# Kernel tuning notes

Hardware: AMD Instinct MI355X
Metric: run time of the kernel (lower is better)

## Reference

```python
import jax, jax.numpy as jnp
import numpy as np

L = 0.24          # lambda step size
K = 0.03          # exp(log 0.03), conductance scale used by forward
NITER = 500       # ctor Niter
DEPS = 0.1


def _g(x, k):
    # Perona-Malik conductance: 1 / (1 + |x^2| / k^2); x real so |x*x| == x*x
    return 1.0 / (1.0 + (x * x) / (k * k))


def setup_inputs() -> dict:
    key = jax.random.key(0)
    k1, k2 = jax.random.split(key)
    guide = jax.random.normal(k1, (2, 3, 512, 512), dtype=jnp.float32)
    initial = jax.random.uniform(k2, (2, 1, 512, 512), dtype=jnp.float32)
    return {"guide": guide, "initial": initial}


def reference(guide, initial):
    # shift branch (jit-safe): forward adds deps if initial.min() <= deps, subtracts at end
    shift = jnp.where(jnp.min(initial) <= DEPS, DEPS, 0.0).astype(initial.dtype)
    depth0 = initial + shift

    # conductance coefficients from guide (mean abs channel gradient), shapes:
    # cv: [B,1,H-1,W], ch: [B,1,H,W-1]
    cv = _g(jnp.mean(jnp.abs(guide[:, :, 1:, :] - guide[:, :, :-1, :]), axis=1, keepdims=True), K)
    ch = _g(jnp.mean(jnp.abs(guide[:, :, :, 1:] - guide[:, :, :, :-1]), axis=1, keepdims=True), K)

    def step(I, _):
        # both diffs computed from the same I (matches torch: dv, dh read before writes;
        # the in-place +/- updates commute, so functional adds give identical math)
        dv = I[:, :, 1:, :] - I[:, :, :-1, :]
        dh = I[:, :, :, 1:] - I[:, :, :, :-1]
        tv = L * cv * dv
        th = L * ch * dh
        I = I.at[:, :, 1:, :].add(-tv)
        I = I.at[:, :, :-1, :].add(tv)
        I = I.at[:, :, :, 1:].add(-th)
        I = I.at[:, :, :, :-1].add(th)
        return I, None

    depth, _ = jax.lax.scan(step, depth0, None, length=NITER)
    y_pred = depth - shift
    return (y_pred, cv, ch)
```

## Files before the change

### kernel.cpp

```cpp
#include <hip/hip_runtime.h>


#define HH 512
#define WW 512
#define NB 2
static constexpr float LAM   = 0.24f;
static constexpr float KCOND = 0.03f;
static constexpr float DEPS_ = 0.1f;
static constexpr int IMG      = HH * WW;
static constexpr int N_DEPTH  = NB * IMG;
static constexpr int CV_PER_B = (HH - 1) * WW;
static constexpr int CH_PER_B = HH * (WW - 1);
static constexpr int N_CV     = NB * CV_PER_B;
static constexpr int N_CH     = NB * CH_PER_B;

static constexpr int T_FUSE = 10, NSS = 50;
static constexpr int TILE_W = 64, TILE_H = 32;
static constexpr int HALO_X = 12, HALO_Y = 10;
static constexpr int RW = TILE_W + 2 * HALO_X;
static constexpr int RH = TILE_H + 2 * HALO_Y;
static constexpr int NQ_ROW = RW / 4;
static constexpr int NQUAD  = NQ_ROW * RH;
static constexpr int SSZ    = (RH + 2) * RW;

static constexpr int NU_ROW = RW / 4;
static constexpr int NU_COL = RH / 2;
static constexpr int NUNIT  = NU_ROW * NU_COL;
static constexpr int NTF    = 576;

static constexpr int S_LDS    = 92;
static constexpr int ROWS_SZ  = (RH + 2) * S_LDS;
static constexpr int TRASH_OFF = ROWS_SZ;
static constexpr int EDGE_OFF = ROWS_SZ + S_LDS;
static constexpr int EDGE_ENT = 580;
static constexpr int BUF_SZ   = EDGE_OFF + EDGE_ENT * 4;
static constexpr int MIN_SCR  = TRASH_OFF + 40;

static constexpr int QPT_F = 5;

__device__ __forceinline__ float2 cohload8(const float* p) {
    unsigned long long u = __hip_atomic_load(
        reinterpret_cast<const unsigned long long*>(p),
        __ATOMIC_RELAXED, __HIP_MEMORY_SCOPE_AGENT);
    union { unsigned long long u; float2 f; } c; c.u = u;
    return c.f;
}
__device__ __forceinline__ void cohstore8(float* p, float a, float b) {
    union { unsigned long long u; float f[2]; } c;
    c.f[0] = a; c.f[1] = b;
    __hip_atomic_store(reinterpret_cast<unsigned long long*>(p), c.u,
                       __ATOMIC_RELAXED, __HIP_MEMORY_SCOPE_AGENT);
}

static constexpr int NCO_BLK = (N_CV + N_CH + 255) / 256;
__global__ void coeff_min_kernel(const float* __restrict__ g,
                                 const float* __restrict__ ini,
                                 float* __restrict__ cv, float* __restrict__ chh,
                                 float* __restrict__ partials,
                                 unsigned* __restrict__ flags) {
    constexpr float kk = KCOND * KCOND;
    if ((int)blockIdx.x >= NCO_BLK) {
        int bid = blockIdx.x - NCO_BLK;
        if (threadIdx.x == 0) flags[bid] = 0u;
        float m = 3.4e38f;
        for (int idx = bid * 256 + threadIdx.x; idx < N_DEPTH; idx += 256 * 256)
            m = fminf(m, ini[idx]);
        for (int off = 32; off > 0; off >>= 1) m = fminf(m, __shfl_down(m, off, 64));
        __shared__ float sm[4];
        int lane = threadIdx.x & 63, wv = threadIdx.x >> 6;
        if (lane == 0) sm[wv] = m;
        __syncthreads();
        if (threadIdx.x == 0)
            partials[bid] = fminf(fminf(sm[0], sm[1]), fminf(sm[2], sm[3]));
        return;
    }
    int idx = blockIdx.x * 256 + threadIdx.x;
    if (idx < N_CV) {
        int b = idx / CV_PER_B;
        int r = idx - b * CV_PER_B;
        int i = r >> 9, j = r & (WW - 1);
        const float* gb = g + b * 3 * IMG + i * WW + j;
        float s = 0.f;
#pragma unroll
        for (int c = 0; c < 3; ++c) s += fabsf(gb[c * IMG + WW] - gb[c * IMG]);
        float m = s / 3.0f;
        cv[idx] = 1.0f / (1.0f + (m * m) / kk);
    } else if (idx < N_CV + N_CH) {
        int t = idx - N_CV;
        int b = t / CH_PER_B;
        int r = t - b * CH_PER_B;
        int i = r / (WW - 1);
        int j = r - i * (WW - 1);
        const float* gb = g + b * 3 * IMG + i * WW + j;
        float s = 0.f;
#pragma unroll
        for (int c = 0; c < 3; ++c) s += fabsf(gb[c * IMG + 1] - gb[c * IMG]);
        float m = s / 3.0f;
        chh[t] = 1.0f / (1.0f + (m * m) / kk);
    }
}

__global__ void key_from_partials(const float* __restrict__ partials,
                                  float* __restrict__ keyf) {
    float m = partials[threadIdx.x];
    for (int off = 32; off > 0; off >>= 1) m = fminf(m, __shfl_down(m, off, 64));
    __shared__ float sm[4];
    int lane = threadIdx.x & 63, wv = threadIdx.x >> 6;
    if (lane == 0) sm[wv] = m;
    __syncthreads();
    if (threadIdx.x == 0)
        keyf[0] = fminf(fminf(sm[0], sm[1]), fminf(sm[2], sm[3]));
}

__global__ __launch_bounds__(NTF, 1) void diffuse_persist(
    const float* __restrict__ initial, float* __restrict__ out_y,
    float* __restrict__ bufA, float* __restrict__ bufB,
    const float* __restrict__ cv_g, const float* __restrict__ ch_g,
    const float* __restrict__ partials, unsigned* __restrict__ flags) {
    __shared__ float sb[2][BUF_SZ];
    const int blk = blockIdx.x;
    const int b   = blk >> 7, t = blk & 127;
    const int ty  = t >> 3, tx = t & 7;
    const int y0  = ty * TILE_H;
    const int x0  = tx * TILE_W;
    const int tid = threadIdx.x;

    const bool act = tid < NUNIT;
    const int  uc  = act ? tid : 0;
    const int  pr  = uc / NU_ROW;
    const int  px  = uc - pr * NU_ROW;
    const int  x   = px * 4;
    const int  r0  = 2 * pr, r1 = r0 + 1;
    int roff0 = (r0 + 1) * S_LDS + x;
    int roff1 = roff0 + S_LDS;
    if (!act) { roff0 = TRASH_OFF + (tid & 3) * 8; roff1 = roff0 + 4; }
    const int e_w  = EDGE_OFF + (tid + 1) * 4;
    const int e_lf = EDGE_OFF + tid * 4 + 2;
    const int e_rt = EDGE_OFF + (tid + 2) * 4;

    const int gy0 = y0 - HALO_Y + r0, gy1 = gy0 + 1;
    const int gx  = x0 - HALO_X + x;
    const bool gx_in = (gx >= 0) && (gx <= WW - 4);
    const bool in0 = act && gx_in && (gy0 >= 0) && (gy0 < HH);
    const bool in1 = act && gx_in && (gy1 >= 0) && (gy1 < HH);
    const int goff0 = in0 ? (gy0 * WW + gx) : 0;
    const int goff1 = in1 ? (gy1 * WW + gx) : 0;
    const bool is_int = act && (r0 >= HALO_Y) && (r1 < HALO_Y + TILE_H) &&
                        (x >= HALO_X) && (x < HALO_X + TILE_W);
    const int rel_r = r0 - HALO_Y, rel_x = x - HALO_X;
    const bool is_inner = is_int && (rel_r >= 10) && (rel_r <= 20) &&
                          (rel_x >= 12) && (rel_x <= 48);
    const bool store_seam = is_int && !is_inner;

    const float* cvb = cv_g + b * CV_PER_B;
    const float* chb = ch_g + b * CH_PER_B;
    float ca[4], cm[4], cb[4], h0[5], h1[5];
#pragma unroll
    for (int j = 0; j < 4; ++j) {
        int gxx = gx + j;
        bool gxo = (gxx >= 0) && (gxx < WW);
        bool a_ok = act && (r0 >= 1) && (gy0 >= 1) && (gy0 <= HH - 1) && gxo;
        ca[j] = a_ok ? LAM * cvb[(gy0 - 1) * WW + gxx] : 0.f;
        bool m_ok = act && (gy1 >= 1) && (gy1 <= HH - 1) && gxo;
        cm[j] = m_ok ? LAM * cvb[(gy1 - 1) * WW + gxx] : 0.f;
        bool b_ok = act && (r1 <= RH - 2) && (gy1 + 1 >= 1) && (gy1 + 1 <= HH - 1) && gxo;
        cb[j] = b_ok ? LAM * cvb[gy1 * WW + gxx] : 0.f;
    }
#pragma unroll
    for (int jj = 0; jj < 5; ++jj) {
        int xe = x + jj, gxe = gx + jj;
        bool e_ok = (xe >= 1) && (xe <= RW - 1) && (gxe >= 1) && (gxe < WW);
        bool ok0 = act && e_ok && (gy0 >= 0) && (gy0 < HH);
        h0[jj] = ok0 ? LAM * chb[gy0 * (WW - 1) + (gxe - 1)] : 0.f;
        bool ok1 = act && e_ok && (gy1 >= 0) && (gy1 < HH);
        h1[jj] = ok1 ? LAM * chb[gy1 * (WW - 1) + (gxe - 1)] : 0.f;
    }

    int nbr = -1;
    if (tid < 8) {
        int d  = tid + (tid >= 4 ? 1 : 0);
        int dy = d / 3 - 1, dx = d % 3 - 1;
        int ny = ty + dy, nx = tx + dx;
        if (ny >= 0 && ny < 16 && nx >= 0 && nx < 8)
            nbr = (b << 7) + (ny << 3) + nx;
    }

    float v0[4] = {0.f, 0.f, 0.f, 0.f}, v1[4] = {0.f, 0.f, 0.f, 0.f};
    const float* ib = initial + b * IMG;
    if (in0) {
        float4 tv = *reinterpret_cast<const float4*>(ib + goff0);
        v0[0] = tv.x; v0[1] = tv.y; v0[2] = tv.z; v0[3] = tv.w;
    }
    if (in1) {
        float4 tv = *reinterpret_cast<const float4*>(ib + goff1);
        v1[0] = tv.x; v1[1] = tv.y; v1[2] = tv.z; v1[3] = tv.w;
    }

    {
        float pm = 3.4e38f;
        if (tid < 256) pm = partials[tid];
        for (int off = 32; off > 0; off >>= 1)
            pm = fminf(pm, __shfl_down(pm, off, 64));
        if (tid < 256 && (tid & 63) == 0) sb[0][MIN_SCR + (tid >> 6)] = pm;
    }

    for (int i = tid; i < S_LDS; i += NTF) {
        sb[0][i] = 0.f; sb[0][(RH + 1) * S_LDS + i] = 0.f;
        sb[1][i] = 0.f; sb[1][(RH + 1) * S_LDS + i] = 0.f;
    }
    if (tid == 0) {
        float4 z{0.f, 0.f, 0.f, 0.f};
        *reinterpret_cast<float4*>(&sb[0][EDGE_OFF]) = z;
        *reinterpret_cast<float4*>(&sb[1][EDGE_OFF]) = z;
        *reinterpret_cast<float4*>(&sb[0][EDGE_OFF + 577 * 4]) = z;
        *reinterpret_cast<float4*>(&sb[1][EDGE_OFF + 577 * 4]) = z;
    }
    __syncthreads();

    const float mm = fminf(fminf(sb[0][MIN_SCR], sb[0][MIN_SCR + 1]),
                           fminf(sb[0][MIN_SCR + 2], sb[0][MIN_SCR + 3]));
    const float shift = (mm <= DEPS_) ? DEPS_ : 0.f;
    if (in0) { v0[0] += shift; v0[1] += shift; v0[2] += shift; v0[3] += shift; }
    if (in1) { v1[0] += shift; v1[1] += shift; v1[2] += shift; v1[3] += shift; }

    *reinterpret_cast<float4*>(&sb[0][roff0]) = float4{v0[0], v0[1], v0[2], v0[3]};
    *reinterpret_cast<float4*>(&sb[0][roff1]) = float4{v1[0], v1[1], v1[2], v1[3]};
    *reinterpret_cast<float4*>(&sb[0][e_w])   = float4{v0[0], v1[0], v0[3], v1[3]};
    __syncthreads();

    for (int k = 0; k < NSS; ++k) {
        if (k > 0) {
            if (nbr >= 0) {
                while (__hip_atomic_load(&flags[nbr], __ATOMIC_RELAXED,
                                         __HIP_MEMORY_SCOPE_AGENT) < (unsigned)k) {}
            }
            __syncthreads();
            asm volatile("" ::: "memory");
            const float* srcb = ((k & 1) ? bufA : bufB) + b * IMG;
            if (act && !is_int) {
                float2 a0{0.f, 0.f}, b0{0.f, 0.f}, a1{0.f, 0.f}, b1{0.f, 0.f};
                if (in0) { a0 = cohload8(srcb + goff0); b0 = cohload8(srcb + goff0 + 2); }
                if (in1) { a1 = cohload8(srcb + goff1); b1 = cohload8(srcb + goff1 + 2); }
                v0[0] = a0.x; v0[1] = a0.y; v0[2] = b0.x; v0[3] = b0.y;
                v1[0] = a1.x; v1[1] = a1.y; v1[2] = b1.x; v1[3] = b1.y;
                *reinterpret_cast<float4*>(&sb[0][roff0]) =
                    float4{v0[0], v0[1], v0[2], v0[3]};
                *reinterpret_cast<float4*>(&sb[0][roff1]) =
                    float4{v1[0], v1[1], v1[2], v1[3]};
                *reinterpret_cast<float4*>(&sb[0][e_w]) =
                    float4{v0[0], v1[0], v0[3], v1[3]};
            }
            __syncthreads();
        }

        int cur = 0;
        for (int it = 0; it < T_FUSE; ++it) {
            const float* s = sb[cur];
            float2 lfp = *reinterpret_cast<const float2*>(&s[e_lf]);
            float2 rtp = *reinterpret_cast<const float2*>(&s[e_rt]);
            float4 up = *reinterpret_cast<const float4*>(&s[roff0 - S_LDS]);
            float4 dn = *reinterpret_cast<const float4*>(&s[roff1 + S_LDS]);

            float n0[4], n1[4];
            n0[0] = v0[0] - ca[0] * (v0[0] - up.x) + cm[0] * (v1[0] - v0[0])
                          - h0[0] * (v0[0] - lfp.x) + h0[1] * (v0[1] - v0[0]);
            n0[1] = v0[1] - ca[1] * (v0[1] - up.y) + cm[1] * (v1[1] - v0[1])
                          - h0[1] * (v0[1] - v0[0]) + h0[2] * (v0[2] - v0[1]);
            n0[2] = v0[2] - ca[2] * (v0[2] - up.z) + cm[2] * (v1[2] - v0[2])
                          - h0[2] * (v0[2] - v0[1]) + h0[3] * (v0[3] - v0[2]);
            n0[3] = v0[3] - ca[3] * (v0[3] - up.w) + cm[3] * (v1[3] - v0[3])
                          - h0[3] * (v0[3] - v0[2]) + h0[4] * (rtp.x - v0[3]);
            n1[0] = v1[0] - cm[0] * (v1[0] - v0[0]) + cb[0] * (dn.x - v1[0])
                          - h1[0] * (v1[0] - lfp.y) + h1[1] * (v1[1] - v1[0]);
            n1[1] = v1[1] - cm[1] * (v1[1] - v0[1]) + cb[1] * (dn.y - v1[1])
                          - h1[1] * (v1[1] - v1[0]) + h1[2] * (v1[2] - v1[1]);
            n1[2] = v1[2] - cm[2] * (v1[2] - v0[2]) + cb[2] * (dn.z - v1[2])
                          - h1[2] * (v1[2] - v1[1]) + h1[3] * (v1[3] - v1[2]);
            n1[3] = v1[3] - cm[3] * (v1[3] - v0[3]) + cb[3] * (dn.w - v1[3])
                          - h1[3] * (v1[3] - v1[2]) + h1[4] * (rtp.y - v1[3]);

            int nxt = cur ^ 1;
            float* d = sb[nxt];
            *reinterpret_cast<float4*>(&d[roff0]) = float4{n0[0], n0[1], n0[2], n0[3]};
            *reinterpret_cast<float4*>(&d[roff1]) = float4{n1[0], n1[1], n1[2], n1[3]};
            *reinterpret_cast<float4*>(&d[e_w])   = float4{n0[0], n1[0], n0[3], n1[3]};
            v0[0] = n0[0]; v0[1] = n0[1]; v0[2] = n0[2]; v0[3] = n0[3];
            v1[0] = n1[0]; v1[1] = n1[1]; v1[2] = n1[2]; v1[3] = n1[3];
            cur = nxt;
            __syncthreads();
        }

        if (k == NSS - 1) {
            float* dstb = out_y + b * IMG;
            if (is_int) {
                float4 o0{v0[0] - shift, v0[1] - shift, v0[2] - shift, v0[3] - shift};
                float4 o1{v1[0] - shift, v1[1] - shift, v1[2] - shift, v1[3] - shift};
                *reinterpret_cast<float4*>(dstb + goff0) = o0;
                *reinterpret_cast<float4*>(dstb + goff1) = o1;
            }
        } else {
            float* dstb = ((k & 1) ? bufB : bufA) + b * IMG;
            if (store_seam) {
                cohstore8(dstb + goff0,     v0[0], v0[1]);
                cohstore8(dstb + goff0 + 2, v0[2], v0[3]);
                cohstore8(dstb + goff1,     v1[0], v1[1]);
                cohstore8(dstb + goff1 + 2, v1[2], v1[3]);
            }
            asm volatile("s_waitcnt vmcnt(0)" ::: "memory");
            __syncthreads();
            if (tid == 0)
                __hip_atomic_store(&flags[blk], (unsigned)(k + 1),
                                   __ATOMIC_RELAXED, __HIP_MEMORY_SCOPE_AGENT);
        }
    }
}

template <bool ADD_SHIFT, bool SUB_SHIFT>
__global__ __launch_bounds__(256, 1) void step_fused(
    const float* __restrict__ src, float* __restrict__ dst,
    const float* __restrict__ cv_g, const float* __restrict__ ch_g,
    const float* __restrict__ keyf) {
    __shared__ float sb[2][SSZ];
    const int blk = blockIdx.x;
    const int b = blk >> 7, t = blk & 127;
    const int y0 = (t >> 3) * TILE_H, x0 = (t & 7) * TILE_W;
    const float* cvb = cv_g + b * CV_PER_B;
    const float* chb = ch_g + b * CH_PER_B;
    const float* srcb = src + b * IMG;
    float* dstb = dst + b * IMG;
    float shift = 0.f;
    if (ADD_SHIFT || SUB_SHIFT) shift = (keyf[0] <= DEPS_) ? DEPS_ : 0.f;
    const int tid = threadIdx.x;
    float v[QPT_F][4], cu[QPT_F][4], cd[QPT_F][4], chq[QPT_F][5];
    int roff[QPT_F], rr[QPT_F], xx[QPT_F];
    bool act[QPT_F];
#pragma unroll
    for (int q = 0; q < QPT_F; ++q) {
        int qi = tid + q * 256;
        act[q] = qi < NQUAD;
        int qc = act[q] ? qi : 0;
        int r = qc / NQ_ROW;
        int x = (qc - r * NQ_ROW) * 4;
        rr[q] = r; xx[q] = x;
        roff[q] = (r + 1) * RW + x;
        int gy = y0 - HALO_Y + r, gx = x0 - HALO_X + x;
        bool gy_in = (gy >= 0) && (gy < HH);
#pragma unroll
        for (int j = 0; j < 4; ++j) {
            int gxx = gx + j;
            bool gx_in = (gxx >= 0) && (gxx < WW);
            bool vin = act[q] && gy_in && gx_in;
            float val = vin ? srcb[gy * WW + gxx] : 0.f;
            if (ADD_SHIFT) val += shift;
            v[q][j] = vin ? val : 0.f;
            bool up_ok = act[q] && (r >= 1) && (gy >= 1) && (gy < HH) && gx_in;
            cu[q][j] = up_ok ? LAM * cvb[(gy - 1) * WW + gxx] : 0.f;
            bool dn_ok = act[q] && (r <= RH - 2) && (gy >= 0) && (gy < HH - 1) && gx_in;
            cd[q][j] = dn_ok ? LAM * cvb[gy * WW + gxx] : 0.f;
        }
#pragma unroll
        for (int jj = 0; jj < 5; ++jj) {
            int xe = x + jj, gxe = gx + jj;
            bool ok = act[q] && (xe >= 1) && (xe <= RW - 1) && gy_in &&
                      (gxe >= 1) && (gxe < WW);
            chq[q][jj] = ok ? LAM * chb[gy * (WW - 1) + (gxe - 1)] : 0.f;
        }
    }
    for (int i = tid; i < RW; i += 256) {
        sb[0][i] = 0.f; sb[0][(RH + 1) * RW + i] = 0.f;
        sb[1][i] = 0.f; sb[1][(RH + 1) * RW + i] = 0.f;
    }
#pragma unroll
    for (int q = 0; q < QPT_F; ++q)
        if (act[q])
            *reinterpret_cast<float4*>(&sb[0][roff[q]]) =
                float4{v[q][0], v[q][1], v[q][2], v[q][3]};
    __syncthreads();
    int cur = 0;
    for (int it = 0; it < T_FUSE; ++it) {
        float nv[QPT_F][4];
#pragma unroll
        for (int q = 0; q < QPT_F; ++q) {
            const float* s = sb[cur];
            float4 up = *reinterpret_cast<const float4*>(&s[roff[q] - RW]);
            float4 dn = *reinterpret_cast<const float4*>(&s[roff[q] + RW]);
            float lf = s[roff[q] - 1];
            float rt = s[roff[q] + 4];
            float c0 = v[q][0], c1 = v[q][1], c2 = v[q][2], c3 = v[q][3];
            nv[q][0] = c0 - cu[q][0] * (c0 - up.x) + cd[q][0] * (dn.x - c0)
                          - chq[q][0] * (c0 - lf) + chq[q][1] * (c1 - c0);
            nv[q][1] = c1 - cu[q][1] * (c1 - up.y) + cd[q][1] * (dn.y - c1)
                          - chq[q][1] * (c1 - c0) + chq[q][2] * (c2 - c1);
            nv[q][2] = c2 - cu[q][2] * (c2 - up.z) + cd[q][2] * (dn.z - c2)
                          - chq[q][2] * (c2 - c1) + chq[q][3] * (c3 - c2);
            nv[q][3] = c3 - cu[q][3] * (c3 - up.w) + cd[q][3] * (dn.w - c3)
                          - chq[q][3] * (c3 - c2) + chq[q][4] * (rt - c3);
        }
        int nxt = cur ^ 1;
#pragma unroll
        for (int q = 0; q < QPT_F; ++q) {
            if (act[q])
                *reinterpret_cast<float4*>(&sb[nxt][roff[q]]) =
                    float4{nv[q][0], nv[q][1], nv[q][2], nv[q][3]};
            v[q][0] = nv[q][0]; v[q][1] = nv[q][1];
            v[q][2] = nv[q][2]; v[q][3] = nv[q][3];
        }
        cur = nxt;
        __syncthreads();
    }
#pragma unroll
    for (int q = 0; q < QPT_F; ++q) {
        if (!act[q]) continue;
        int r = rr[q], x = xx[q];
        if (r >= HALO_Y && r < HALO_Y + TILE_H && x >= HALO_X && x < HALO_X + TILE_W) {
            int gy = y0 - HALO_Y + r, gx = x0 - HALO_X + x;
            float4 o{v[q][0], v[q][1], v[q][2], v[q][3]};
            if (SUB_SHIFT) { o.x -= shift; o.y -= shift; o.z -= shift; o.w -= shift; }
            *reinterpret_cast<float4*>(dstb + gy * WW + gx) = o;
        }
    }
}

extern "C" void kernel_launch(void* const* d_in, const int* in_sizes, int n_in,
                              void* d_out, int out_size, void* d_ws, size_t ws_size,
                              hipStream_t stream) {
    const float* guide   = (const float*)d_in[0];
    const float* initial = (const float*)d_in[1];
    float* out    = (float*)d_out;
    float* out_y  = out;
    float* out_cv = out + N_DEPTH;
    float* out_ch = out + N_DEPTH + N_CV;

    float* wsf    = (float*)d_ws;
    float* keyf   = wsf;
    float* bufA   = wsf + 64;
    float* bufB   = bufA + N_DEPTH;
    unsigned* flags = (unsigned*)(bufB + N_DEPTH);
    float* partials = (float*)(flags + 256);

    const size_t need = (size_t)(64 + 2 * N_DEPTH + 512) * 4;
    const bool fast = ws_size >= need;

    hipLaunchKernelGGL(coeff_min_kernel, dim3(NCO_BLK + 256), dim3(256), 0, stream,
                       guide, initial, out_cv, out_ch, partials, flags);

    if (fast) {
        hipLaunchKernelGGL(diffuse_persist, dim3(256), dim3(NTF), 0, stream,
                           initial, out_y, bufA, bufB, out_cv, out_ch,
                           partials, flags);
        return;
    }

    hipLaunchKernelGGL(key_from_partials, dim3(1), dim3(256), 0, stream,
                       partials, keyf);
    float* bufs[2] = {bufA, bufB};
    for (int k = 0; k < NSS; ++k) {
        const float* src = (k == 0) ? initial : bufs[(k + 1) & 1];
        float*       dst = (k == NSS - 1) ? out_y : bufs[k & 1];
        if (k == 0)
            hipLaunchKernelGGL((step_fused<true, false>), dim3(256), dim3(256), 0,
                               stream, src, dst, out_cv, out_ch, keyf);
        else if (k == NSS - 1)
            hipLaunchKernelGGL((step_fused<false, true>), dim3(256), dim3(256), 0,
                               stream, src, dst, out_cv, out_ch, keyf);
        else
            hipLaunchKernelGGL((step_fused<false, false>), dim3(256), dim3(256), 0,
                               stream, src, dst, out_cv, out_ch, keyf);
    }
}
```

Measured before the change: 442.1 us.

## Replace per-block neighbor spin with per-thread owner-flag waits and early seam stores

Before, eight lanes spun on the flags of the eight neighbouring blocks, followed by a block-wide barrier. Now each halo-loading thread spins only on the flag of the block that owns its pixels and loads as soon as that block is ready, which removes one barrier per super-step. Seam values are written to global memory during the last fused iteration instead of after it, and the final intra-loop barrier is dropped. In exchange, many threads spin on global flags at once, and correctness now depends on the owner-block mapping and on the memory ordering of the remaining barriers.

```diff
diff --git a/kernel.cpp b/kernel.cpp
--- a/kernel.cpp
+++ b/kernel.cpp
@@ -152,6 +152,13 @@
                           (rel_x >= 12) && (rel_x <= 48);
     const bool store_seam = is_int && !is_inner;
 
+    const bool reload = act && !is_int && (in0 || in1);
+    int pblk = 0;
+    if (reload) {
+        int gyy = in0 ? gy0 : gy1;
+        pblk = (b << 7) + ((gyy >> 5) << 3) + (gx >> 6);
+    }
+
     const float* cvb = cv_g + b * CV_PER_B;
     const float* chb = ch_g + b * CH_PER_B;
     float ca[4], cm[4], cb[4], h0[5], h1[5];
@@ -176,15 +183,6 @@
         h1[jj] = ok1 ? LAM * chb[gy1 * (WW - 1) + (gxe - 1)] : 0.f;
     }
 
-    int nbr = -1;
-    if (tid < 8) {
-        int d  = tid + (tid >= 4 ? 1 : 0);
-        int dy = d / 3 - 1, dx = d % 3 - 1;
-        int ny = ty + dy, nx = tx + dx;
-        if (ny >= 0 && ny < 16 && nx >= 0 && nx < 8)
-            nbr = (b << 7) + (ny << 3) + nx;
-    }
-
     float v0[4] = {0.f, 0.f, 0.f, 0.f}, v1[4] = {0.f, 0.f, 0.f, 0.f};
     const float* ib = initial + b * IMG;
     if (in0) {
@@ -230,14 +228,11 @@
 
     for (int k = 0; k < NSS; ++k) {
         if (k > 0) {
-            if (nbr >= 0) {
-                while (__hip_atomic_load(&flags[nbr], __ATOMIC_RELAXED,
+            if (reload) {
+                while (__hip_atomic_load(&flags[pblk], __ATOMIC_RELAXED,
                                          __HIP_MEMORY_SCOPE_AGENT) < (unsigned)k) {}
-            }
-            __syncthreads();
-            asm volatile("" ::: "memory");
-            const float* srcb = ((k & 1) ? bufA : bufB) + b * IMG;
-            if (act && !is_int) {
+                asm volatile("" ::: "memory");
+                const float* srcb = ((k & 1) ? bufA : bufB) + b * IMG;
                 float2 a0{0.f, 0.f}, b0{0.f, 0.f}, a1{0.f, 0.f}, b1{0.f, 0.f};
                 if (in0) { a0 = cohload8(srcb + goff0); b0 = cohload8(srcb + goff0 + 2); }
                 if (in1) { a1 = cohload8(srcb + goff1); b1 = cohload8(srcb + goff1 + 2); }
@@ -252,6 +247,9 @@
             }
             __syncthreads();
         }
+
+        const bool do_seam = store_seam && (k < NSS - 1);
+        float* dst_sb = ((k & 1) ? bufB : bufA) + b * IMG;
 
         int cur = 0;
         for (int it = 0; it < T_FUSE; ++it) {
@@ -279,6 +277,13 @@
             n1[3] = v1[3] - cm[3] * (v1[3] - v0[3]) + cb[3] * (dn.w - v1[3])
                           - h1[3] * (v1[3] - v1[2]) + h1[4] * (rtp.y - v1[3]);
 
+            if (it == T_FUSE - 1 && do_seam) {
+                cohstore8(dst_sb + goff0,     n0[0], n0[1]);
+                cohstore8(dst_sb + goff0 + 2, n0[2], n0[3]);
+                cohstore8(dst_sb + goff1,     n1[0], n1[1]);
+                cohstore8(dst_sb + goff1 + 2, n1[2], n1[3]);
+            }
+
             int nxt = cur ^ 1;
             float* d = sb[nxt];
             *reinterpret_cast<float4*>(&d[roff0]) = float4{n0[0], n0[1], n0[2], n0[3]};
@@ -287,7 +292,7 @@
             v0[0] = n0[0]; v0[1] = n0[1]; v0[2] = n0[2]; v0[3] = n0[3];
             v1[0] = n1[0]; v1[1] = n1[1]; v1[2] = n1[2]; v1[3] = n1[3];
             cur = nxt;
-            __syncthreads();
+            if (it != T_FUSE - 1) __syncthreads();
         }
 
         if (k == NSS - 1) {
@@ -299,13 +304,6 @@
                 *reinterpret_cast<float4*>(dstb + goff1) = o1;
             }
         } else {
-            float* dstb = ((k & 1) ? bufB : bufA) + b * IMG;
-            if (store_seam) {
-                cohstore8(dstb + goff0,     v0[0], v0[1]);
-                cohstore8(dstb + goff0 + 2, v0[2], v0[3]);
-                cohstore8(dstb + goff1,     v1[0], v1[1]);
-                cohstore8(dstb + goff1 + 2, v1[2], v1[3]);
-            }
             asm volatile("s_waitcnt vmcnt(0)" ::: "memory");
             __syncthreads();
             if (tid == 0)
```

Measured after the change: 439.4 us. No clear change (-0.6%).
